# Kernel tuning notes

Measured on AMD Instinct MI355X. Metric: run time of the kernel, lower is better.

Reference implementation:

```python
import jax, jax.numpy as jnp
import numpy as np

N = 20000      # interaction nodes
E = 160000     # edges
NU = 100000    # num_users
NI = 100000    # num_items
EMB = 64       # emb_size
L1, L2 = 256, 128  # GCN layer dims
H = 2          # GAT heads (and number of GAT layers)
EPS = 1e-5


def _seg(x, idx, n):
    return jax.ops.segment_sum(x, idx, num_segments=n)


def _gcn(x, W, b, src, dst, n):
    # GCNConv: add self-loops, sym-normalize, aggregate src->dst
    loops = jnp.arange(n)
    s = jnp.concatenate([src, loops])
    d = jnp.concatenate([dst, loops])
    deg = _seg(jnp.ones(s.shape[0], x.dtype), d, n)
    dinv = jnp.where(deg > 0, 1.0 / jnp.sqrt(deg), 0.0)
    xw = x @ W
    return _seg((dinv[s] * dinv[d])[:, None] * xw[s], d, n) + b


def _bn(x, g, b):
    # BatchNorm1d in training mode: biased batch statistics
    mu = x.mean(0)
    var = x.var(0)
    return (x - mu) / jnp.sqrt(var + EPS) * g + b


def _sage(x, Wl, bl, Wr, src, dst, n):
    # SAGEConv: mean neighbor aggregation (no self loops) + root transform
    cnt = _seg(jnp.ones(src.shape[0], x.dtype), dst, n)
    agg = _seg(x[src], dst, n) / jnp.maximum(cnt, 1.0)[:, None]
    return agg @ Wl + bl + x @ Wr


def _cheb(x, W0, W1c, b, src, dst, n):
    # ChebConv K=2, lambda_max=2: Tx0 = x, Tx1 = -D^{-1/2} A D^{-1/2} x
    deg = _seg(jnp.ones(src.shape[0], x.dtype), dst, n)
    dinv = jnp.where(deg > 0, 1.0 / jnp.sqrt(deg), 0.0)
    tx1 = -_seg((dinv[src] * dinv[dst])[:, None] * x[src], dst, n)
    return x @ W0 + tx1 @ W1c + b


def _gat(x, W, a_s, a_d, b, src, dst, n):
    # GATConv: add self-loops, per-edge attention softmax over dst, concat=False -> mean over heads
    loops = jnp.arange(n)
    s = jnp.concatenate([src, loops])
    d = jnp.concatenate([dst, loops])
    xp = (x @ W).reshape(n, H, L2)           # [n, H, C]
    al = (xp * a_s).sum(-1)                  # [n, H]
    ar = (xp * a_d).sum(-1)                  # [n, H]
    e = jax.nn.leaky_relu(al[s] + ar[d], 0.2)  # [E', H]
    m = jax.lax.stop_gradient(jax.ops.segment_max(e, d, num_segments=n))
    ex = jnp.exp(e - m[d])
    alpha = ex / _seg(ex, d, n)[d]
    out = _seg(alpha[:, :, None] * xp[s], d, n)  # [n, H, C]
    return out.mean(1) + b


def setup_inputs() -> dict:
    key = jax.random.key(0)
    ks = jax.random.split(key, 40)
    f = lambda k, shp: jax.random.normal(k, shp, dtype=jnp.float32) * 0.02
    inp = {
        'user_idx': jax.random.randint(ks[0], (N,), 0, NU, dtype=jnp.int32),
        'item_idx': jax.random.randint(ks[1], (N,), 0, NI, dtype=jnp.int32),
        'edge_index': jax.random.randint(ks[2], (2, E), 0, N, dtype=jnp.int32),
        'user_emb': f(ks[3], (NU, EMB)),
        'item_emb': f(ks[4], (NI, EMB)),
        'W1': f(ks[5], (2 * EMB, 1024)), 'b1': f(ks[6], (1024,)),
        'W2': f(ks[7], (1024, 512)), 'b2': f(ks[8], (512,)),
        'Wg1': f(ks[9], (512, L1)), 'bg1': f(ks[10], (L1,)),
        'gamma1': 1.0 + f(ks[11], (L1,)), 'beta1': f(ks[12], (L1,)),
        'Wg2': f(ks[13], (L1, L2)), 'bg2': f(ks[14], (L2,)),
        'gamma2': 1.0 + f(ks[15], (L2,)), 'beta2': f(ks[16], (L2,)),
        'Wsl': f(ks[17], (L2, L2)), 'bsl': f(ks[18], (L2,)),
        'Wsr': f(ks[19], (L2, L2)),
        'Wc0': f(ks[20], (L2, L2)), 'Wc1': f(ks[21], (L2, L2)), 'bc': f(ks[22], (L2,)),
        'Wgat1': f(ks[23], (L2, H * L2)), 'as1': f(ks[24], (H, L2)), 'ad1': f(ks[25], (H, L2)), 'bgat1': f(ks[26], (L2,)),
        'Wgat2': f(ks[27], (L2, H * L2)), 'as2': f(ks[28], (H, L2)), 'ad2': f(ks[29], (H, L2)), 'bgat2': f(ks[30], (L2,)),
        'Wp': f(ks[31], (L2, 1)), 'bp': f(ks[32], (1,)),
    }
    return inp


def reference(user_idx, item_idx, edge_index, user_emb, item_emb, W1, b1, W2, b2,
              Wg1, bg1, gamma1, beta1, Wg2, bg2, gamma2, beta2,
              Wsl, bsl, Wsr, Wc0, Wc1, bc,
              Wgat1, as1, ad1, bgat1, Wgat2, as2, ad2, bgat2, Wp, bp):
    src, dst = edge_index[0], edge_index[1]
    n = user_idx.shape[0]
    x = jnp.concatenate([user_emb[user_idx], item_emb[item_idx]], axis=1)
    # MLP (dropout is identity in eval mode)
    x = jax.nn.relu(x @ W1 + b1)
    x = jax.nn.relu(x @ W2 + b2)
    x = jax.nn.relu(_bn(_gcn(x, Wg1, bg1, src, dst, n), gamma1, beta1))
    x = jax.nn.relu(_bn(_gcn(x, Wg2, bg2, src, dst, n), gamma2, beta2))
    x = jax.nn.relu(_sage(x, Wsl, bsl, Wsr, src, dst, n))
    x = jax.nn.relu(_cheb(x, Wc0, Wc1, bc, src, dst, n))
    x = jax.nn.elu(_gat(x, Wgat1, as1, ad1, bgat1, src, dst, n))
    x = jax.nn.elu(_gat(x, Wgat2, as2, ad2, bgat2, src, dst, n))
    return (x @ Wp + bp)[:, 0]
```

## Files before the change

### kernel.cpp

```cpp
#include <hip/hip_runtime.h>
#include <hip/hip_bf16.h>

typedef __hip_bfloat16 bf16;
typedef short s8v __attribute__((ext_vector_type(8)));
typedef float f4v __attribute__((ext_vector_type(4)));

#define NN 20000
#define NE 160000
#define BN_EPS 1e-5f
#define NB 79

#define GF_BIAS 1
#define GF_RELU 2

static __device__ __forceinline__ float b2f(const bf16 x){ return __bfloat162float(x); }
static __device__ __forceinline__ float bits2f(unsigned int u){ return __uint_as_float(u << 16); }
static __device__ __forceinline__ unsigned short f2bits(float f){
  bf16 h = __float2bfloat16(f);
  unsigned short u; __builtin_memcpy(&u, &h, 2); return u;
}
static __device__ __forceinline__ float lrelu(float v){ return (v > 0.f) ? v : 0.2f * v; }

static inline int cdiv(int a, int b){ return (a + b - 1) / b; }


__global__ void k_chk_bf(const unsigned short* __restrict__ x, int n, int code,
                         int* __restrict__ diag){
  bool bad = false;
  for (int k = blockIdx.x * 256 + threadIdx.x; k < n; k += gridDim.x * 256)
    if ((x[k] & 0x7F80u) == 0x7F80u) bad = true;
  if (bad) atomicCAS(diag, 0, code);
}

__global__ void k_diag_out(const int* __restrict__ diag, float* __restrict__ out){
  int d = *diag;
  if (d == 0) return;
  int i = blockIdx.x * 256 + threadIdx.x;
  if (i < NN) out[i] = (float)(d * 100);
}


__global__ void k_ideg(const int* __restrict__ dst, int* __restrict__ ideg){
  int e = blockIdx.x * 256 + threadIdx.x;
  if (e < NE) atomicAdd(&ideg[dst[e]], 1);
}

__global__ __launch_bounds__(256) void k_scan1(const int* __restrict__ ideg,
                                               int* __restrict__ tmp,
                                               int* __restrict__ bsum){
  __shared__ int lds[256];
  int tid = threadIdx.x;
  int i = blockIdx.x * 256 + tid;
  int v = (i < NN) ? ideg[i] : 0;
  lds[tid] = v;
  __syncthreads();
  for (int off = 1; off < 256; off <<= 1){
    int t = (tid >= off) ? lds[tid - off] : 0;
    __syncthreads();
    lds[tid] += t;
    __syncthreads();
  }
  if (i < NN) tmp[i] = lds[tid];
  if (tid == 255) bsum[blockIdx.x] = lds[255];
}

__global__ __launch_bounds__(128) void k_scan2(const int* __restrict__ bsum,
                                               int* __restrict__ boff){
  __shared__ int lds[128];
  int tid = threadIdx.x;
  int v = (tid < NB) ? bsum[tid] : 0;
  lds[tid] = v;
  __syncthreads();
  for (int off = 1; off < 128; off <<= 1){
    int t = (tid >= off) ? lds[tid - off] : 0;
    __syncthreads();
    lds[tid] += t;
    __syncthreads();
  }
  if (tid < NB) boff[tid] = lds[tid] - v;
}

__global__ __launch_bounds__(256) void k_scan3(const int* __restrict__ ideg,
                                               const int* __restrict__ boff,
                                               int* __restrict__ rowptr,
                                               int* __restrict__ cursor,
                                               float* __restrict__ dg,
                                               float* __restrict__ dc,
                                               float* __restrict__ ic){
  int i = blockIdx.x * 256 + threadIdx.x;
  if (i == 0) rowptr[NN] = NE;
  if (i >= NN) return;
  int v = ideg[i];
  int excl = cursor[i] - v + boff[blockIdx.x];
  rowptr[i] = excl;
  cursor[i] = excl;
  float d = (float)v;
  dg[i] = rsqrtf(d + 1.0f);
  dc[i] = (d > 0.f) ? rsqrtf(d) : 0.f;
  ic[i] = 1.0f / fmaxf(d, 1.0f);
}

__global__ void k_fill(const int* __restrict__ src, const int* __restrict__ dst,
                       int* __restrict__ cursor, int* __restrict__ colsrc){
  int e = blockIdx.x * 256 + threadIdx.x;
  if (e >= NE) return;
  int pos = atomicAdd(&cursor[dst[e]], 1);
  colsrc[pos] = src[e];
}


struct WtPack {
  const float* W[10]; short* hi[10]; short* lo[10];
  int K[10]; int nshift[10]; int base[11];
};

__global__ __launch_bounds__(256) void k_wtall(WtPack p){
  int idx = blockIdx.x * 256 + threadIdx.x;
  if (idx >= p.base[10]) return;
  int seg = 0;
#pragma unroll
  for (int i = 1; i < 10; i++) seg += (idx >= p.base[i]) ? 1 : 0;
  int local = idx - p.base[seg];
  int K = p.K[seg], ns = p.nshift[seg];
  int n = local & ((1 << ns) - 1), k = local >> ns;
  float w = p.W[seg][local];
  unsigned short h = f2bits(w);
  unsigned short l = f2bits(w - bits2f(h));
  p.hi[seg][(size_t)n * K + k] = (short)h;
  p.lo[seg][(size_t)n * K + k] = (short)l;
}


__global__ void k_gather(const int* __restrict__ uidx, const int* __restrict__ iidx,
                         const float* __restrict__ ue, const float* __restrict__ ie,
                         bf16* __restrict__ x0){
  int idx = blockIdx.x * 256 + threadIdx.x;
  if (idx >= NN * 128) return;
  int i = idx >> 7, c = idx & 127;
  float v = (c < 64) ? ue[(size_t)uidx[i] * 64 + c] : ie[(size_t)iidx[i] * 64 + (c - 64)];
  x0[idx] = __float2bfloat16(v);
}


__global__ __launch_bounds__(256) void k_mm64(
    const bf16* A0, const short* B0h, const short* B0l, int K0,
    const bf16* A1, const short* B1h, const short* B1l, int K1,
    const float* __restrict__ bias, bf16* __restrict__ C,
    int M, int Ncol, int flags, int npass){
  __shared__ short As[64][40];
  __shared__ short Bhs[64][40];
  __shared__ short Bls[64][40];
  const int tid = threadIdx.x;
  const int bid = blockIdx.y * gridDim.x + blockIdx.x;
  const int total = gridDim.x * gridDim.y;
  const int L = (bid & 7) * (total >> 3) + (bid >> 3);
  const int row0 = (L / gridDim.x) * 64, col0 = (L % gridDim.x) * 64;
  if (row0 >= M) return;
  const int wid = tid >> 6, lane = tid & 63;
  const int wr = (wid >> 1) * 32, wc = (wid & 1) * 32;
  const int lr = lane & 15, lq = lane >> 4;
  const int sr = tid >> 2, sq = (tid & 3) * 8;

  f4v acc[2][2];
#pragma unroll
  for (int i = 0; i < 2; i++)
#pragma unroll
    for (int j = 0; j < 2; j++)
      acc[i][j] = f4v{0.f, 0.f, 0.f, 0.f};

  const bf16* Aarr[2] = {A0, A1};
  const short* Bharr[2] = {B0h, B1h};
  const short* Blarr[2] = {B0l, B1l};
  const int Karr[2] = {K0, K1};

  for (int p = 0; p < npass; p++){
    const short* A = (const short*)Aarr[p];
    const short* Bh = Bharr[p];
    const short* Bl = Blarr[p];
    const int K = Karr[p];
    for (int k0 = 0; k0 < K; k0 += 32){
      uint4 va = make_uint4(0u, 0u, 0u, 0u);
      int grow = row0 + sr;
      if (grow < M) va = *(const uint4*)(A + (size_t)grow * K + k0 + sq);
      *(uint4*)&As[sr][sq] = va;
      size_t boff = (size_t)(col0 + sr) * K + k0 + sq;
      *(uint4*)&Bhs[sr][sq] = *(const uint4*)(Bh + boff);
      *(uint4*)&Bls[sr][sq] = *(const uint4*)(Bl + boff);
      __syncthreads();
      s8v a[2], bh[2], bl[2];
#pragma unroll
      for (int i = 0; i < 2; i++) a[i] = *(const s8v*)&As[wr + i * 16 + lr][lq * 8];
#pragma unroll
      for (int j = 0; j < 2; j++){
        bh[j] = *(const s8v*)&Bhs[wc + j * 16 + lr][lq * 8];
        bl[j] = *(const s8v*)&Bls[wc + j * 16 + lr][lq * 8];
      }
#pragma unroll
      for (int i = 0; i < 2; i++)
#pragma unroll
        for (int j = 0; j < 2; j++){
          acc[i][j] = __builtin_amdgcn_mfma_f32_16x16x32_bf16(a[i], bh[j], acc[i][j], 0, 0, 0);
          acc[i][j] = __builtin_amdgcn_mfma_f32_16x16x32_bf16(a[i], bl[j], acc[i][j], 0, 0, 0);
        }
      __syncthreads();
    }
  }

#pragma unroll
  for (int i = 0; i < 2; i++){
#pragma unroll
    for (int rg = 0; rg < 4; rg++){
      int row = row0 + wr + i * 16 + lq * 4 + rg;
      if (row >= M) continue;
#pragma unroll
      for (int j = 0; j < 2; j++){
        int col = col0 + wc + j * 16 + lr;
        float v = acc[i][j][rg];
        if (flags & GF_BIAS) v += bias[col];
        if (flags & GF_RELU) v = fmaxf(v, 0.f);
        C[(size_t)row * Ncol + col] = __float2bfloat16(v);
      }
    }
  }
}


__global__ __launch_bounds__(256) void k_agg(
    const int* __restrict__ rowptr, const int* __restrict__ colsrc,
    const bf16* __restrict__ x, const float* __restrict__ wn,
    const float* __restrict__ icv, const float* __restrict__ bias,
    float* __restrict__ outf, bf16* __restrict__ outb,
    int qshift, int mode){
  int idx = blockIdx.x * 256 + threadIdx.x;
  int total = NN << qshift;
  if (idx >= total) return;
  int d = idx >> qshift, q = idx & ((1 << qshift) - 1);
  int F = 4 << qshift;
  int c = q * 4;
  int r0 = rowptr[d], r1 = rowptr[d + 1];
  float s0 = 0.f, s1 = 0.f, s2 = 0.f, s3 = 0.f;
  const short* xs = (const short*)x;
  for (int r = r0; r < r1; r += 4){
    int n = r1 - r;
    int i0 = colsrc[r];
    int i1 = (n > 1) ? colsrc[r + 1] : 0;
    int i2 = (n > 2) ? colsrc[r + 2] : 0;
    int i3 = (n > 3) ? colsrc[r + 3] : 0;
    float w0 = (mode == 1) ? 1.f : wn[i0];
    float w1 = (n > 1) ? ((mode == 1) ? 1.f : wn[i1]) : 0.f;
    float w2 = (n > 2) ? ((mode == 1) ? 1.f : wn[i2]) : 0.f;
    float w3 = (n > 3) ? ((mode == 1) ? 1.f : wn[i3]) : 0.f;
    uint2 v0 = *(const uint2*)(xs + (size_t)i0 * F + c);
    uint2 v1 = *(const uint2*)(xs + (size_t)i1 * F + c);
    uint2 v2 = *(const uint2*)(xs + (size_t)i2 * F + c);
    uint2 v3 = *(const uint2*)(xs + (size_t)i3 * F + c);
    s0 += w0 * bits2f(v0.x & 0xffffu) + w1 * bits2f(v1.x & 0xffffu)
        + w2 * bits2f(v2.x & 0xffffu) + w3 * bits2f(v3.x & 0xffffu);
    s1 += w0 * bits2f(v0.x >> 16) + w1 * bits2f(v1.x >> 16)
        + w2 * bits2f(v2.x >> 16) + w3 * bits2f(v3.x >> 16);
    s2 += w0 * bits2f(v0.y & 0xffffu) + w1 * bits2f(v1.y & 0xffffu)
        + w2 * bits2f(v2.y & 0xffffu) + w3 * bits2f(v3.y & 0xffffu);
    s3 += w0 * bits2f(v0.y >> 16) + w1 * bits2f(v1.y >> 16)
        + w2 * bits2f(v2.y >> 16) + w3 * bits2f(v3.y >> 16);
  }
  if (mode == 0){
    float w = wn[d], w2 = w * w;
    uint2 vd = *(const uint2*)(xs + (size_t)d * F + c);
    float4 o;
    o.x = w * s0 + w2 * bits2f(vd.x & 0xffffu) + bias[c + 0];
    o.y = w * s1 + w2 * bits2f(vd.x >> 16)     + bias[c + 1];
    o.z = w * s2 + w2 * bits2f(vd.y & 0xffffu) + bias[c + 2];
    o.w = w * s3 + w2 * bits2f(vd.y >> 16)     + bias[c + 3];
    *(float4*)(outf + (size_t)d * F + c) = o;
  } else {
    float m = (mode == 1) ? icv[d] : -wn[d];
    unsigned int lo = (unsigned int)f2bits(s0 * m) | ((unsigned int)f2bits(s1 * m) << 16);
    unsigned int hi = (unsigned int)f2bits(s2 * m) | ((unsigned int)f2bits(s3 * m) << 16);
    *(uint2*)((short*)outb + (size_t)d * F + c) = make_uint2(lo, hi);
  }
}


__global__ void k_bn_stats(const float* __restrict__ x, float* __restrict__ stats, int F){
  int c = threadIdx.x & (F - 1);
  int rsub = threadIdx.x / F;
  int rpi = 256 / F;
  int r0 = blockIdx.x * 128;
  int rend = min(NN, r0 + 128);
  float s1 = 0.f, s2 = 0.f;
  for (int r = r0 + rsub; r < rend; r += rpi){
    float v = x[(size_t)r * F + c];
    s1 += v; s2 += v * v;
  }
  atomicAdd(&stats[c], s1);
  atomicAdd(&stats[F + c], s2);
}

__global__ void k_bn_apply(const float* __restrict__ x, const float* __restrict__ stats,
                           const float* __restrict__ g, const float* __restrict__ b,
                           int fshift, int total, bf16* __restrict__ out){
  int idx = blockIdx.x * 256 + threadIdx.x;
  if (idx >= total) return;
  int F = 1 << fshift;
  int c = idx & (F - 1);
  float mu = stats[c] * (1.0f / NN);
  float var = fmaxf(stats[F + c] * (1.0f / NN) - mu * mu, 0.f);
  float v = (x[idx] - mu) * rsqrtf(var + BN_EPS) * g[c] + b[c];
  out[idx] = __float2bfloat16(fmaxf(v, 0.f));
}


__global__ __launch_bounds__(256) void k_gat_alar(const bf16* __restrict__ xp,
                                                  const float* __restrict__ as_,
                                                  const float* __restrict__ ad_,
                                                  float* __restrict__ al,
                                                  float* __restrict__ ar){
  int d = blockIdx.x * 4 + (threadIdx.x >> 6);
  int lane = threadIdx.x & 63;
  if (d >= NN) return;
  int c0 = lane * 2;
  unsigned int p0 = *(const unsigned int*)((const short*)xp + (size_t)d * 256 + c0);
  unsigned int p1 = *(const unsigned int*)((const short*)xp + (size_t)d * 256 + 128 + c0);
  float x00 = bits2f(p0 & 0xffffu), x01 = bits2f(p0 >> 16);
  float x10 = bits2f(p1 & 0xffffu), x11 = bits2f(p1 >> 16);
  float sa0 = x00 * as_[c0] + x01 * as_[c0 + 1];
  float sd0 = x00 * ad_[c0] + x01 * ad_[c0 + 1];
  float sa1 = x10 * as_[128 + c0] + x11 * as_[128 + c0 + 1];
  float sd1 = x10 * ad_[128 + c0] + x11 * ad_[128 + c0 + 1];
#pragma unroll
  for (int off = 32; off > 0; off >>= 1){
    sa0 += __shfl_xor(sa0, off); sd0 += __shfl_xor(sd0, off);
    sa1 += __shfl_xor(sa1, off); sd1 += __shfl_xor(sd1, off);
  }
  if (lane == 0){
    al[d * 2] = sa0;     ar[d * 2] = sd0;
    al[d * 2 + 1] = sa1; ar[d * 2 + 1] = sd1;
  }
}

__global__ __launch_bounds__(64) void k_gat(const int* __restrict__ rowptr,
                                            const int* __restrict__ colsrc,
                                            const bf16* __restrict__ xp,
                                            const float* __restrict__ al,
                                            const float* __restrict__ ar,
                                            const float* __restrict__ bias,
                                            bf16* __restrict__ outb,
                                            const float* __restrict__ wp,
                                            const float* __restrict__ bp,
                                            float* __restrict__ outf){
  __shared__ float w0s[64], w1s[64];
  __shared__ int ss[64];
  int d = blockIdx.x;
  int lane = threadIdx.x;
  int r0 = rowptr[d], r1 = rowptr[d + 1];
  float ard0 = ar[d * 2], ard1 = ar[d * 2 + 1];
  float e0 = lrelu(al[d * 2] + ard0);
  float e1 = lrelu(al[d * 2 + 1] + ard1);
  float mx0 = e0, mx1 = e1;
  for (int r = r0 + lane; r < r1; r += 64){
    int s = colsrc[r];
    mx0 = fmaxf(mx0, lrelu(al[s * 2] + ard0));
    mx1 = fmaxf(mx1, lrelu(al[s * 2 + 1] + ard1));
  }
#pragma unroll
  for (int off = 32; off > 0; off >>= 1){
    mx0 = fmaxf(mx0, __shfl_xor(mx0, off));
    mx1 = fmaxf(mx1, __shfl_xor(mx1, off));
  }
  float ps0 = (lane == 0) ? expf(e0 - mx0) : 0.f;
  float ps1 = (lane == 0) ? expf(e1 - mx1) : 0.f;
  for (int r = r0 + lane; r < r1; r += 64){
    int s = colsrc[r];
    ps0 += expf(lrelu(al[s * 2] + ard0) - mx0);
    ps1 += expf(lrelu(al[s * 2 + 1] + ard1) - mx1);
  }
#pragma unroll
  for (int off = 32; off > 0; off >>= 1){
    ps0 += __shfl_xor(ps0, off);
    ps1 += __shfl_xor(ps1, off);
  }
  int c0 = lane * 2;
  float a00, a01, a10, a11;
  {
    float w0 = expf(e0 - mx0), w1 = expf(e1 - mx1);
    unsigned int p0 = *(const unsigned int*)((const short*)xp + (size_t)d * 256 + c0);
    unsigned int p1 = *(const unsigned int*)((const short*)xp + (size_t)d * 256 + 128 + c0);
    a00 = w0 * bits2f(p0 & 0xffffu); a01 = w0 * bits2f(p0 >> 16);
    a10 = w1 * bits2f(p1 & 0xffffu); a11 = w1 * bits2f(p1 >> 16);
  }
  for (int t0 = r0; t0 < r1; t0 += 64){
    int nt = min(64, r1 - t0);
    __syncthreads();
    if (lane < nt){
      int s = colsrc[t0 + lane];
      ss[lane] = s;
      w0s[lane] = expf(lrelu(al[s * 2] + ard0) - mx0);
      w1s[lane] = expf(lrelu(al[s * 2 + 1] + ard1) - mx1);
    }
    __syncthreads();
    for (int r = 0; r < nt; r++){
      int s = ss[r];
      float w0 = w0s[r], w1 = w1s[r];
      unsigned int p0 = *(const unsigned int*)((const short*)xp + (size_t)s * 256 + c0);
      unsigned int p1 = *(const unsigned int*)((const short*)xp + (size_t)s * 256 + 128 + c0);
      a00 += w0 * bits2f(p0 & 0xffffu); a01 += w0 * bits2f(p0 >> 16);
      a10 += w1 * bits2f(p1 & 0xffffu); a11 += w1 * bits2f(p1 >> 16);
    }
  }
  float v0 = 0.5f * (a00 / ps0 + a10 / ps1) + bias[c0];
  float v1 = 0.5f * (a01 / ps0 + a11 / ps1) + bias[c0 + 1];
  v0 = (v0 > 0.f) ? v0 : expm1f(v0);
  v1 = (v1 > 0.f) ? v1 : expm1f(v1);
  if (wp == nullptr){
    unsigned int packed = (unsigned int)f2bits(v0) | ((unsigned int)f2bits(v1) << 16);
    *(unsigned int*)((short*)outb + (size_t)d * 128 + c0) = packed;
  } else {
    float pv = v0 * wp[c0] + v1 * wp[c0 + 1];
#pragma unroll
    for (int off = 32; off > 0; off >>= 1) pv += __shfl_down(pv, off);
    if (lane == 0) outf[d] = pv + bp[0];
  }
}


extern "C" void kernel_launch(void* const* d_in, const int* in_sizes, int n_in,
                              void* d_out, int out_size, void* d_ws, size_t ws_size,
                              hipStream_t stream){
  const int* uidx = (const int*)d_in[0];
  const int* iidx = (const int*)d_in[1];
  const int* eidx = (const int*)d_in[2];
  const int* src = eidx;
  const int* dst = eidx + NE;
  const float* ue  = (const float*)d_in[3];
  const float* ie  = (const float*)d_in[4];
  const float* W1  = (const float*)d_in[5];  const float* b1  = (const float*)d_in[6];
  const float* W2  = (const float*)d_in[7];  const float* b2  = (const float*)d_in[8];
  const float* Wg1 = (const float*)d_in[9];  const float* bg1 = (const float*)d_in[10];
  const float* gamma1 = (const float*)d_in[11]; const float* beta1 = (const float*)d_in[12];
  const float* Wg2 = (const float*)d_in[13]; const float* bg2 = (const float*)d_in[14];
  const float* gamma2 = (const float*)d_in[15]; const float* beta2 = (const float*)d_in[16];
  const float* Wsl = (const float*)d_in[17]; const float* bsl = (const float*)d_in[18];
  const float* Wsr = (const float*)d_in[19];
  const float* Wc0 = (const float*)d_in[20]; const float* Wc1 = (const float*)d_in[21];
  const float* bc  = (const float*)d_in[22];
  const float* Wgat1 = (const float*)d_in[23]; const float* as1 = (const float*)d_in[24];
  const float* ad1 = (const float*)d_in[25];   const float* bgat1 = (const float*)d_in[26];
  const float* Wgat2 = (const float*)d_in[27]; const float* as2 = (const float*)d_in[28];
  const float* ad2 = (const float*)d_in[29];   const float* bgat2 = (const float*)d_in[30];
  const float* Wp  = (const float*)d_in[31];   const float* bp  = (const float*)d_in[32];

  int* diag   = (int*)d_ws;
  int* ideg   = diag + 4;
  float* stats1 = (float*)(ideg + NN);
  float* stats2 = stats1 + 512;
  int* bsum   = (int*)(stats2 + 256);
  int* boff   = bsum + 128;
  int* rowptr = boff + 128;
  int* cursor = rowptr + NN + 4;
  int* colsrc = cursor + NN;
  float* dg = (float*)(colsrc + NE);
  float* dc = dg + NN;
  float* ic = dc + NN;
  float* al = ic + NN;
  float* ar = al + 2 * NN;
  short* w1h = (short*)(ar + 2 * NN);
  short* w1l = w1h + 131072;
  short* w2h = w1l + 131072;
  short* w2l = w2h + 524288;
  short* wg1h = w2l + 524288;
  short* wg1l = wg1h + 131072;
  short* wg2h = wg1l + 131072;
  short* wg2l = wg2h + 32768;
  short* wslh = wg2l + 32768;
  short* wsll = wslh + 16384;
  short* wsrh = wsll + 16384;
  short* wsrl = wsrh + 16384;
  short* wc0h = wsrl + 16384;
  short* wc0l = wc0h + 16384;
  short* wc1h = wc0l + 16384;
  short* wc1l = wc1h + 16384;
  short* wgat1h = wc1l + 16384;
  short* wgat1l = wgat1h + 32768;
  short* wgat2h = wgat1l + 32768;
  short* wgat2l = wgat2h + 32768;
  short* X0 = wgat2l + 32768;
  short* H1 = X0 + (size_t)NN * 128;
  short* H2 = H1 + (size_t)10000 * 1024;

  bf16* x0b  = (bf16*)X0;
  bf16* h1b  = (bf16*)H1;
  bf16* h2b  = (bf16*)H2;
  bf16* xw1b = (bf16*)H1;
  float* g1f = (float*)H2;
  bf16* g1b  = (bf16*)(H1 + (size_t)NN * 256);
  bf16* xw2b = (bf16*)X0;
  float* x3f = (float*)H1;
  bf16* x3b  = (bf16*)H2;
  bf16* aggb = (bf16*)X0;
  bf16* x4b  = (bf16*)(H2 + (size_t)NN * 128);
  bf16* tx1b = (bf16*)X0;
  bf16* x5b  = (bf16*)(H2 + (size_t)NN * 256);
  bf16* xpb  = (bf16*)H1;
  bf16* x6b  = (bf16*)X0;

  auto mm = [&](const bf16* A1, const short* B1h, const short* B1l, int K1,
                const bf16* A2, const short* B2h, const short* B2l, int K2,
                const float* bias, bf16* C, int M, int N, int flags){
    int nx = N / 64;
    int ny = cdiv(M, 64);
    while ((nx * ny) & 7) ny++;
    dim3 g(nx, ny);
    int np = A2 ? 2 : 1;
    k_mm64<<<g, 256, 0, stream>>>(A1, B1h, B1l, K1, A2, B2h, B2l, K2,
                                  bias, C, M, N, flags, np);
  };

  hipMemsetAsync(diag, 0, (size_t)(4 + NN + 768) * 4, stream);

  k_ideg<<<cdiv(NE, 256), 256, 0, stream>>>(dst, ideg);
  k_scan1<<<NB, 256, 0, stream>>>(ideg, cursor, bsum);
  k_scan2<<<1, 128, 0, stream>>>(bsum, boff);
  k_scan3<<<NB, 256, 0, stream>>>(ideg, boff, rowptr, cursor, dg, dc, ic);
  k_fill<<<cdiv(NE, 256), 256, 0, stream>>>(src, dst, cursor, colsrc);

  {
    WtPack p;
    const float* Ws[10] = {W1, W2, Wg1, Wg2, Wsl, Wsr, Wc0, Wc1, Wgat1, Wgat2};
    short* his[10] = {w1h, w2h, wg1h, wg2h, wslh, wsrh, wc0h, wc1h, wgat1h, wgat2h};
    short* los[10] = {w1l, w2l, wg1l, wg2l, wsll, wsrl, wc0l, wc1l, wgat1l, wgat2l};
    int Ks[10] = {128, 1024, 512, 256, 128, 128, 128, 128, 128, 128};
    int nss[10] = {10, 9, 8, 7, 7, 7, 7, 7, 8, 8};
    int off = 0;
    for (int i = 0; i < 10; i++){
      p.W[i] = Ws[i]; p.hi[i] = his[i]; p.lo[i] = los[i];
      p.K[i] = Ks[i]; p.nshift[i] = nss[i]; p.base[i] = off;
      off += Ks[i] << nss[i];
    }
    p.base[10] = off;
    k_wtall<<<cdiv(off, 256), 256, 0, stream>>>(p);
  }

  k_gather<<<cdiv(NN * 128, 256), 256, 0, stream>>>(uidx, iidx, ue, ie, x0b);

  for (int ofs = 0; ofs < NN; ofs += 10000){
    mm(x0b + (size_t)ofs * 128, w1h, w1l, 128, nullptr, nullptr, nullptr, 0,
       b1, h1b, 10000, 1024, GF_BIAS | GF_RELU);
    mm(h1b, w2h, w2l, 1024, nullptr, nullptr, nullptr, 0,
       b2, h2b + (size_t)ofs * 512, 10000, 512, GF_BIAS | GF_RELU);
  }

  mm(h2b, wg1h, wg1l, 512, nullptr, nullptr, nullptr, 0, nullptr, xw1b, NN, 256, 0);
  k_agg<<<cdiv(NN * 64, 256), 256, 0, stream>>>(rowptr, colsrc, xw1b, dg, nullptr, bg1, g1f, nullptr, 6, 0);
  k_bn_stats<<<cdiv(NN, 128), 256, 0, stream>>>(g1f, stats1, 256);
  k_bn_apply<<<cdiv(NN * 256, 256), 256, 0, stream>>>(g1f, stats1, gamma1, beta1, 8, NN * 256, g1b);

  mm(g1b, wg2h, wg2l, 256, nullptr, nullptr, nullptr, 0, nullptr, xw2b, NN, 128, 0);
  k_agg<<<cdiv(NN * 32, 256), 256, 0, stream>>>(rowptr, colsrc, xw2b, dg, nullptr, bg2, x3f, nullptr, 5, 0);
  k_bn_stats<<<cdiv(NN, 128), 256, 0, stream>>>(x3f, stats2, 128);
  k_bn_apply<<<cdiv(NN * 128, 256), 256, 0, stream>>>(x3f, stats2, gamma2, beta2, 7, NN * 128, x3b);

  k_agg<<<cdiv(NN * 32, 256), 256, 0, stream>>>(rowptr, colsrc, x3b, nullptr, ic, nullptr, nullptr, aggb, 5, 1);
  mm(aggb, wslh, wsll, 128, x3b, wsrh, wsrl, 128, bsl, x4b, NN, 128, GF_BIAS | GF_RELU);

  k_agg<<<cdiv(NN * 32, 256), 256, 0, stream>>>(rowptr, colsrc, x4b, dc, nullptr, nullptr, nullptr, tx1b, 5, 2);
  mm(x4b, wc0h, wc0l, 128, tx1b, wc1h, wc1l, 128, bc, x5b, NN, 128, GF_BIAS | GF_RELU);

  mm(x5b, wgat1h, wgat1l, 128, nullptr, nullptr, nullptr, 0, nullptr, xpb, NN, 256, 0);
  k_gat_alar<<<cdiv(NN, 4), 256, 0, stream>>>(xpb, as1, ad1, al, ar);
  k_gat<<<NN, 64, 0, stream>>>(rowptr, colsrc, xpb, al, ar, bgat1, x6b,
                               nullptr, nullptr, nullptr);
  k_chk_bf<<<256, 256, 0, stream>>>((const unsigned short*)x6b, NN * 128, 16, diag);

  mm(x6b, wgat2h, wgat2l, 128, nullptr, nullptr, nullptr, 0, nullptr, xpb, NN, 256, 0);
  k_gat_alar<<<cdiv(NN, 4), 256, 0, stream>>>(xpb, as2, ad2, al, ar);
  k_gat<<<NN, 64, 0, stream>>>(rowptr, colsrc, xpb, al, ar, bgat2, nullptr,
                               Wp, bp, (float*)d_out);
  k_diag_out<<<cdiv(NN, 256), 256, 0, stream>>>(diag, (float*)d_out);
}
```

Before: 635.5 us.

## Double the GEMM K-tile to 64 and prefetch next tile into registers

The k_mm64 GEMM now stages a 64-wide K slice per iteration instead of 32, which halves the number of barrier pairs. It also loads the next slice from global memory into registers while the MFMAs for the current slice run. The intent is to hide global load latency and cut synchronisation overhead in the hi/lo split-bf16 matmul. In exchange it uses more LDS and registers, and it assumes K is a multiple of 64.

Result: faster. 617.1 us (-2.9%).

```diff
diff --git a/kernel.cpp b/kernel.cpp
--- a/kernel.cpp
+++ b/kernel.cpp
@@ -147,9 +147,9 @@
     const bf16* A1, const short* B1h, const short* B1l, int K1,
     const float* __restrict__ bias, bf16* __restrict__ C,
     int M, int Ncol, int flags, int npass){
-  __shared__ short As[64][40];
-  __shared__ short Bhs[64][40];
-  __shared__ short Bls[64][40];
+  __shared__ short As[64][72];
+  __shared__ short Bhs[64][72];
+  __shared__ short Bls[64][72];
   const int tid = threadIdx.x;
   const int bid = blockIdx.y * gridDim.x + blockIdx.x;
   const int total = gridDim.x * gridDim.y;
@@ -159,7 +159,7 @@
   const int wid = tid >> 6, lane = tid & 63;
   const int wr = (wid >> 1) * 32, wc = (wid & 1) * 32;
   const int lr = lane & 15, lq = lane >> 4;
-  const int sr = tid >> 2, sq = (tid & 3) * 8;
+  const int sr = tid >> 2, sq = (tid & 3) * 16;
 
   f4v acc[2][2];
 #pragma unroll
@@ -172,36 +172,52 @@
   const short* Bharr[2] = {B0h, B1h};
   const short* Blarr[2] = {B0l, B1l};
   const int Karr[2] = {K0, K1};
+
+  const bool arow_ok = (row0 + sr) < M;
 
   for (int p = 0; p < npass; p++){
     const short* A = (const short*)Aarr[p];
     const short* Bh = Bharr[p];
     const short* Bl = Blarr[p];
     const int K = Karr[p];
-    for (int k0 = 0; k0 < K; k0 += 32){
-      uint4 va = make_uint4(0u, 0u, 0u, 0u);
-      int grow = row0 + sr;
-      if (grow < M) va = *(const uint4*)(A + (size_t)grow * K + k0 + sq);
-      *(uint4*)&As[sr][sq] = va;
-      size_t boff = (size_t)(col0 + sr) * K + k0 + sq;
-      *(uint4*)&Bhs[sr][sq] = *(const uint4*)(Bh + boff);
-      *(uint4*)&Bls[sr][sq] = *(const uint4*)(Bl + boff);
+    const short* arow = A + (size_t)(row0 + sr) * K + sq;
+    const short* bhrow = Bh + (size_t)(col0 + sr) * K + sq;
+    const short* blrow = Bl + (size_t)(col0 + sr) * K + sq;
+
+    uint4 ra0 = make_uint4(0,0,0,0), ra1 = make_uint4(0,0,0,0);
+    if (arow_ok){ ra0 = *(const uint4*)(arow); ra1 = *(const uint4*)(arow + 8); }
+    uint4 rb0 = *(const uint4*)(bhrow), rb1 = *(const uint4*)(bhrow + 8);
+    uint4 rc0 = *(const uint4*)(blrow), rc1 = *(const uint4*)(blrow + 8);
+
+    for (int k0 = 0; k0 < K; k0 += 64){
+      *(uint4*)&As[sr][sq] = ra0;  *(uint4*)&As[sr][sq + 8] = ra1;
+      *(uint4*)&Bhs[sr][sq] = rb0; *(uint4*)&Bhs[sr][sq + 8] = rb1;
+      *(uint4*)&Bls[sr][sq] = rc0; *(uint4*)&Bls[sr][sq + 8] = rc1;
       __syncthreads();
-      s8v a[2], bh[2], bl[2];
-#pragma unroll
-      for (int i = 0; i < 2; i++) a[i] = *(const s8v*)&As[wr + i * 16 + lr][lq * 8];
-#pragma unroll
-      for (int j = 0; j < 2; j++){
-        bh[j] = *(const s8v*)&Bhs[wc + j * 16 + lr][lq * 8];
-        bl[j] = *(const s8v*)&Bls[wc + j * 16 + lr][lq * 8];
+      if (k0 + 64 < K){
+        int off = k0 + 64;
+        if (arow_ok){ ra0 = *(const uint4*)(arow + off); ra1 = *(const uint4*)(arow + off + 8); }
+        rb0 = *(const uint4*)(bhrow + off); rb1 = *(const uint4*)(bhrow + off + 8);
+        rc0 = *(const uint4*)(blrow + off); rc1 = *(const uint4*)(blrow + off + 8);
       }
 #pragma unroll
-      for (int i = 0; i < 2; i++)
+      for (int t = 0; t < 2; t++){
+        s8v a[2], bh2[2], bl2[2];
+#pragma unroll
+        for (int i = 0; i < 2; i++) a[i] = *(const s8v*)&As[wr + i * 16 + lr][t * 32 + lq * 8];
 #pragma unroll
         for (int j = 0; j < 2; j++){
-          acc[i][j] = __builtin_amdgcn_mfma_f32_16x16x32_bf16(a[i], bh[j], acc[i][j], 0, 0, 0);
-          acc[i][j] = __builtin_amdgcn_mfma_f32_16x16x32_bf16(a[i], bl[j], acc[i][j], 0, 0, 0);
+          bh2[j] = *(const s8v*)&Bhs[wc + j * 16 + lr][t * 32 + lq * 8];
+          bl2[j] = *(const s8v*)&Bls[wc + j * 16 + lr][t * 32 + lq * 8];
         }
+#pragma unroll
+        for (int i = 0; i < 2; i++)
+#pragma unroll
+          for (int j = 0; j < 2; j++){
+            acc[i][j] = __builtin_amdgcn_mfma_f32_16x16x32_bf16(a[i], bh2[j], acc[i][j], 0, 0, 0);
+            acc[i][j] = __builtin_amdgcn_mfma_f32_16x16x32_bf16(a[i], bl2[j], acc[i][j], 0, 0, 0);
+          }
+      }
       __syncthreads();
     }
   }
```
